# Kernel optimization log

Hardware: AMD Instinct MI355X
Metric: run time of the kernel (lower is better)

Reference implementation:

```python
import jax, jax.numpy as jnp
import numpy as np

B, S, H = 4, 2048, 512
I = 1024  # intermediate_dim
E = 8     # num_experts
K = 2     # top_k


def setup_inputs() -> dict:
    key = jax.random.key(0)
    k1, k2, k3, k4 = jax.random.split(key, 4)
    x = jax.random.normal(k1, (B, S, H), dtype=jnp.float32)
    expert_indices = jax.random.randint(k2, (B, S, K), 0, E, dtype=jnp.int32)
    # parameters: init.normal_(std=0.02)
    w13 = 0.02 * jax.random.normal(k3, (E, H, 2 * I), dtype=jnp.float32)
    w2 = 0.02 * jax.random.normal(k4, (E, I, H), dtype=jnp.float32)
    return {"x": x, "expert_indices": expert_indices, "w13": w13, "w2": w2}


def reference(x, expert_indices, w13, w2):
    # x: (B,S,H); expert_indices: (B,S,K); w13: (E,H,2I); w2: (E,I,H)
    # Same math as torch's per-token weight gather + matmul, expressed as
    # dense all-expert GEMM followed by per-token expert selection.
    h13_all = jnp.einsum('bsh,ehd->bsed', x, w13)          # (B,S,E,2I)
    h13 = jnp.take_along_axis(h13_all, expert_indices[..., None], axis=2)  # (B,S,K,2I)
    gate, up = jnp.split(h13, 2, axis=-1)                   # each (B,S,K,I)
    h_inter = jax.nn.silu(gate) * up                        # (B,S,K,I)
    out_all = jnp.einsum('bski,eih->bskeh', h_inter, w2)    # (B,S,K,E,H)
    out = jnp.take_along_axis(out_all, expert_indices[..., None, None], axis=3)
    return out.squeeze(3)                                   # (B,S,K,H)
```

## Files before the change

kernel.cpp:

```cpp
#include <hip/hip_runtime.h>


#define H_DIM 512
#define I_DIM 1024
#define E_NUM 8
#define P_PAIRS 16384
#define CAP P_PAIRS
#define MAX_TILES 136

#define PREP_TW13 2048
#define PREP_TW2 1024
#define PREP_CVT 2048
#define PREP_ROUTE 64
#define PREP_BLOCKS (PREP_TW13 + PREP_TW2 + PREP_CVT + PREP_ROUTE)

typedef _Float16 half8 __attribute__((ext_vector_type(8)));
typedef _Float16 half4 __attribute__((ext_vector_type(4)));
typedef float f32x4 __attribute__((ext_vector_type(4)));
typedef unsigned int u32;
typedef const __attribute__((address_space(1))) u32* gas_t;
typedef __attribute__((address_space(3))) u32* las_t;

__device__ __forceinline__ void glds16(const void* g, void* l) {
  __builtin_amdgcn_global_load_lds((gas_t)g, (las_t)l, 16, 0, 0);
}

__device__ __forceinline__ bool tile_decode(const int* counts, int ty, int& e,
                                            int& m0, int& ne, int& rb) {
  int base = 0;
  rb = 0;
  for (e = 0; e < E_NUM; ++e) {
    ne = counts[e];
    const int nt = (ne + 127) >> 7;
    if (ty < base + nt) { m0 = (ty - base) << 7; return true; }
    base += nt;
    rb += ne;
  }
  return false;
}

__global__ __launch_bounds__(256) void prep_k(
    const float* __restrict__ x, const int* __restrict__ idx,
    const float* __restrict__ w13, const float* __restrict__ w2,
    int* __restrict__ counts, int* __restrict__ lists,
    _Float16* __restrict__ xh, _Float16* __restrict__ w13t,
    _Float16* __restrict__ w2t) {
  __shared__ __align__(16) _Float16 tile[64][68];
  const int b = blockIdx.x;
  const int tid = threadIdx.x;

  if (b < PREP_TW13 + PREP_TW2) {
    const float* src;
    _Float16* dst;
    int R, C, c0, r0;
    if (b < PREP_TW13) {
      R = H_DIM; C = 2 * I_DIM;
      const int e = b >> 8;
      c0 = (b & 31) * 64;
      r0 = ((b >> 5) & 7) * 64;
      src = w13 + (size_t)e * R * C;
      dst = w13t + (size_t)e * C * R;
    } else {
      const int l = b - PREP_TW13;
      R = I_DIM; C = H_DIM;
      const int e = l >> 7;
      c0 = (l & 7) * 64;
      r0 = ((l >> 3) & 15) * 64;
      src = w2 + (size_t)e * R * C;
      dst = w2t + (size_t)e * C * R;
    }
    {
      const int c4 = (tid & 15) * 4;
      const int r4 = (tid >> 4) * 4;
      f32x4 v[4];
      for (int i = 0; i < 4; ++i)
        v[i] = *(const f32x4*)(src + (size_t)(r0 + r4 + i) * C + c0 + c4);
      for (int j = 0; j < 4; ++j) {
        half4 hv = {(_Float16)v[0][j], (_Float16)v[1][j],
                    (_Float16)v[2][j], (_Float16)v[3][j]};
        *(half4*)&tile[c4 + j][r4] = hv;
      }
    }
    __syncthreads();
    {
      const int c = tid >> 3;
      const int r8 = (tid & 7) * 8;
      for (int pass = 0; pass < 2; ++pass) {
        const int col = pass * 32 + c;
        half4 lo = *(const half4*)&tile[col][r8];
        half4 hi = *(const half4*)&tile[col][r8 + 4];
        half8 h = {lo[0], lo[1], lo[2], lo[3], hi[0], hi[1], hi[2], hi[3]};
        *(half8*)(dst + (size_t)(c0 + col) * R + r0 + r8) = h;
      }
    }
  } else if (b < PREP_TW13 + PREP_TW2 + PREP_CVT) {
    const int l = b - (PREP_TW13 + PREP_TW2);
    const size_t i = ((size_t)l * 256 + tid) * 8;
    f32x4 v0 = *(const f32x4*)(x + i);
    f32x4 v1 = *(const f32x4*)(x + i + 4);
    half8 h;
    for (int j = 0; j < 4; ++j) { h[j] = (_Float16)v0[j]; h[j + 4] = (_Float16)v1[j]; }
    *(half8*)(xh + i) = h;
  } else {
    int* lcnt = (int*)&tile[0][0];
    int* lbase = lcnt + E_NUM;
    const int l = b - (PREP_TW13 + PREP_TW2 + PREP_CVT);
    if (tid < E_NUM) lcnt[tid] = 0;
    __syncthreads();
    const int p = l * 256 + tid;
    const int e = idx[p];
    const int r = atomicAdd(&lcnt[e], 1);
    __syncthreads();
    if (tid < E_NUM) lbase[tid] = atomicAdd(&counts[tid], lcnt[tid]);
    __syncthreads();
    lists[e * CAP + lbase[e] + r] = p;
  }
}

__global__ __launch_bounds__(256) void gemm1_k(
    const _Float16* __restrict__ xh, const _Float16* __restrict__ w13t,
    const int* __restrict__ counts, const int* __restrict__ lists,
    _Float16* __restrict__ h_ws) {
  int e, m0, ne, rb;
  if (!tile_decode(counts, blockIdx.y, e, m0, ne, rb)) return;
  const int n0 = blockIdx.x * 64;

  __shared__ int rows[128];
  __shared__ __align__(16) _Float16 As[128 * 32];
  __shared__ __align__(16) _Float16 Bgs[64 * 32];
  __shared__ __align__(16) _Float16 Bus[64 * 32];

  const int tid = threadIdx.x;
  if (tid < 128) {
    const int m = m0 + tid;
    rows[tid] = (m < ne) ? lists[e * CAP + m] : -1;
  }
  __syncthreads();

  const int sr = tid >> 2;
  const int s4 = tid & 3;
  const int segoff = ((s4 ^ ((sr >> 1) & 3)) * 8);
  const int pa0 = rows[sr];
  const int pa1 = rows[64 + sr];
  const int t0 = (pa0 >= 0) ? (pa0 >> 1) : 0;
  const int t1 = (pa1 >= 0) ? (pa1 >> 1) : 0;
  const _Float16* ga0 = xh + (size_t)t0 * H_DIM + segoff;
  const _Float16* ga1 = xh + (size_t)t1 * H_DIM + segoff;
  const _Float16* gbg = w13t + ((size_t)e * 2 * I_DIM + n0 + sr) * H_DIM + segoff;
  const _Float16* gbu = gbg + (size_t)I_DIM * H_DIM;
  _Float16* la0 = As + sr * 32 + s4 * 8;
  _Float16* la1 = As + (64 + sr) * 32 + s4 * 8;
  _Float16* lbg = Bgs + sr * 32 + s4 * 8;
  _Float16* lbu = Bus + sr * 32 + s4 * 8;

  const int lane = tid & 63;
  const int wid = tid >> 6;
  const int wm = wid & 1;
  const int wn = wid >> 1;
  const int fm = lane & 15;
  const int q = lane >> 4;
  int aoff[4], boff[2];
  for (int mi = 0; mi < 4; ++mi) {
    const int rA = wm * 64 + mi * 16 + fm;
    aoff[mi] = rA * 32 + ((q ^ ((rA >> 1) & 3)) * 8);
  }
  for (int ni = 0; ni < 2; ++ni) {
    const int cB = wn * 32 + ni * 16 + fm;
    boff[ni] = cB * 32 + ((q ^ ((cB >> 1) & 3)) * 8);
  }

  f32x4 accg[4][2] = {};
  f32x4 accu[4][2] = {};

  for (int k0 = 0; k0 < H_DIM; k0 += 32) {
    glds16(ga0 + k0, la0);
    glds16(ga1 + k0, la1);
    glds16(gbg + k0, lbg);
    glds16(gbu + k0, lbu);
    __syncthreads();

    half8 af[4], bg[2], bu[2];
    for (int mi = 0; mi < 4; ++mi) af[mi] = *(const half8*)&As[aoff[mi]];
    for (int ni = 0; ni < 2; ++ni) {
      bg[ni] = *(const half8*)&Bgs[boff[ni]];
      bu[ni] = *(const half8*)&Bus[boff[ni]];
    }
    for (int mi = 0; mi < 4; ++mi)
      for (int ni = 0; ni < 2; ++ni) {
        accg[mi][ni] = __builtin_amdgcn_mfma_f32_16x16x32_f16(af[mi], bg[ni], accg[mi][ni], 0, 0, 0);
        accu[mi][ni] = __builtin_amdgcn_mfma_f32_16x16x32_f16(af[mi], bu[ni], accu[mi][ni], 0, 0, 0);
      }
    __syncthreads();
  }

  for (int mi = 0; mi < 4; ++mi)
    for (int r = 0; r < 4; ++r) {
      const int mrow = wm * 64 + mi * 16 + q * 4 + r;
      if (m0 + mrow >= ne) continue;
      _Float16* hrow = h_ws + (size_t)(rb + m0 + mrow) * I_DIM + n0;
      for (int ni = 0; ni < 2; ++ni) {
        const int c = wn * 32 + ni * 16 + fm;
        const float g = accg[mi][ni][r];
        const float u = accu[mi][ni][r];
        hrow[c] = (_Float16)(g / (1.0f + __expf(-g)) * u);
      }
    }
}

__global__ __launch_bounds__(256) void gemm2_k(
    const _Float16* __restrict__ h_ws, const _Float16* __restrict__ w2t,
    const int* __restrict__ counts, const int* __restrict__ lists,
    float* __restrict__ out) {
  int e, m0, ne, rb;
  if (!tile_decode(counts, blockIdx.x, e, m0, ne, rb)) return;
  const int n0 = blockIdx.y * 64;

  __shared__ int rows[128];
  __shared__ __align__(16) _Float16 As[2][128 * 64];
  __shared__ __align__(16) _Float16 Bs[2][64 * 64];

  const int tid = threadIdx.x;
  if (tid < 128) {
    const int m = m0 + tid;
    rows[tid] = (m < ne) ? lists[e * CAP + m] : -1;
  }

  const int s8 = tid & 7;
  const int sr8 = tid >> 3;
  const int sw = ((s8 ^ (sr8 & 7)) * 8);
  const _Float16* gA[4];
  int lA[4];
  for (int pa = 0; pa < 4; ++pa) {
    const int m = pa * 32 + sr8;
    int grow = rb + m0 + m;
    if (grow > P_PAIRS - 1) grow = P_PAIRS - 1;
    gA[pa] = h_ws + (size_t)grow * I_DIM + sw;
    lA[pa] = m * 64 + s8 * 8;
  }
  const _Float16* gB[2];
  int lB[2];
  for (int pb = 0; pb < 2; ++pb) {
    const int n = pb * 32 + sr8;
    gB[pb] = w2t + ((size_t)e * H_DIM + n0 + n) * I_DIM + sw;
    lB[pb] = n * 64 + s8 * 8;
  }

  const int lane = tid & 63;
  const int wid = tid >> 6;
  const int wm = wid & 1;
  const int wn = wid >> 1;
  const int fm = lane & 15;
  const int q = lane >> 4;
  int aoff[2][4], boff[2][2];
  for (int ks = 0; ks < 2; ++ks) {
    for (int mi = 0; mi < 4; ++mi) {
      const int rA = wm * 64 + mi * 16 + fm;
      aoff[ks][mi] = rA * 64 + (((ks * 4 + q) ^ (rA & 7)) * 8);
    }
    for (int ni = 0; ni < 2; ++ni) {
      const int cB = wn * 32 + ni * 16 + fm;
      boff[ks][ni] = cB * 64 + (((ks * 4 + q) ^ (cB & 7)) * 8);
    }
  }

  f32x4 acc[4][2] = {};

#define G2_STAGE(buf, k0)                                  \
  do {                                                     \
    for (int pa = 0; pa < 4; ++pa)                         \
      glds16(gA[pa] + (k0), &As[buf][lA[pa]]);             \
    for (int pb = 0; pb < 2; ++pb)                         \
      glds16(gB[pb] + (k0), &Bs[buf][lB[pb]]);             \
  } while (0)

#define G2_COMPUTE(buf)                                                          \
  do {                                                                           \
    for (int ks = 0; ks < 2; ++ks) {                                             \
      half8 af[4], bf[2];                                                        \
      for (int mi = 0; mi < 4; ++mi)                                             \
        af[mi] = *(const half8*)&As[buf][aoff[ks][mi]];                          \
      for (int ni = 0; ni < 2; ++ni)                                             \
        bf[ni] = *(const half8*)&Bs[buf][boff[ks][ni]];                          \
      for (int mi = 0; mi < 4; ++mi)                                             \
        for (int ni = 0; ni < 2; ++ni)                                           \
          acc[mi][ni] = __builtin_amdgcn_mfma_f32_16x16x32_f16(                  \
              af[mi], bf[ni], acc[mi][ni], 0, 0, 0);                             \
    }                                                                            \
  } while (0)

  G2_STAGE(0, 0);
  __syncthreads();
  for (int k0 = 0; k0 < I_DIM; k0 += 128) {
    G2_STAGE(1, k0 + 64);
    G2_COMPUTE(0);
    __syncthreads();
    if (k0 + 128 < I_DIM) G2_STAGE(0, k0 + 128);
    G2_COMPUTE(1);
    __syncthreads();
  }
#undef G2_STAGE
#undef G2_COMPUTE

  for (int mi = 0; mi < 4; ++mi)
    for (int r = 0; r < 4; ++r) {
      const int mrow = wm * 64 + mi * 16 + q * 4 + r;
      const int p = rows[mrow];
      if (p < 0) continue;
      float* orow = out + (size_t)p * H_DIM + n0;
      for (int ni = 0; ni < 2; ++ni)
        orow[wn * 32 + ni * 16 + fm] = acc[mi][ni][r];
    }
}

extern "C" void kernel_launch(void* const* d_in, const int* in_sizes, int n_in,
                              void* d_out, int out_size, void* d_ws, size_t ws_size,
                              hipStream_t stream) {
  const float* x = (const float*)d_in[0];
  const int* idx = (const int*)d_in[1];
  const float* w13 = (const float*)d_in[2];
  const float* w2 = (const float*)d_in[3];

  char* ws = (char*)d_ws;
  int* counts = (int*)ws;
  int* lists = (int*)(ws + 2048);
  const size_t OFF_XH = 2048 + (size_t)E_NUM * CAP * 4;
  const size_t OFF_W13T = OFF_XH + (size_t)P_PAIRS / 2 * H_DIM * 2;
  const size_t OFF_W2T = OFF_W13T + (size_t)E_NUM * 2 * I_DIM * H_DIM * 2;
  const size_t OFF_H = OFF_W2T + (size_t)E_NUM * H_DIM * I_DIM * 2;
  _Float16* xh = (_Float16*)(ws + OFF_XH);
  _Float16* w13t = (_Float16*)(ws + OFF_W13T);
  _Float16* w2t = (_Float16*)(ws + OFF_W2T);
  _Float16* h_ws = (_Float16*)(ws + OFF_H);

  hipMemsetAsync(d_ws, 0, 128, stream);
  prep_k<<<dim3(PREP_BLOCKS), 256, 0, stream>>>(x, idx, w13, w2, counts, lists,
                                                xh, w13t, w2t);
  gemm1_k<<<dim3(I_DIM / 64, MAX_TILES), 256, 0, stream>>>(
      xh, w13t, counts, lists, h_ws);
  gemm2_k<<<dim3(MAX_TILES, H_DIM / 64), 256, 0, stream>>>(
      h_ws, w2t, counts, lists, (float*)d_out);
}
```

Before: 201.1 us.

## Overlap w2 transpose with gemm1 and vectorize epilogue stores via swapped MFMA operands

Moves the w2 fp32-to-fp16 transpose out of the prep kernel and into extra gemm1 blocks, so it runs concurrently with the first expert GEMM instead of on the prep critical path. Swaps the MFMA A/B operands so each lane holds four consecutive output columns. That lets the gemm1 SiLU epilogue write half4 vectors and the gemm2 epilogue write float4 vectors instead of scalar stores. The transpose helper also changes its LDS padding and load pattern. This adds idle extra blocks to gemm1 and some shared memory for the tile buffer, which may reduce occupancy.

```diff
diff --git a/kernel.cpp b/kernel.cpp
--- a/kernel.cpp
+++ b/kernel.cpp
@@ -9,10 +9,13 @@
 #define MAX_TILES 136
 
 #define PREP_TW13 2048
-#define PREP_TW2 1024
 #define PREP_CVT 2048
 #define PREP_ROUTE 64
-#define PREP_BLOCKS (PREP_TW13 + PREP_TW2 + PREP_CVT + PREP_ROUTE)
+#define PREP_BLOCKS (PREP_TW13 + PREP_CVT + PREP_ROUTE)
+
+#define G1_NX 16
+#define G1_TW2X 8
+#define TW2_BLOCKS 1024
 
 typedef _Float16 half8 __attribute__((ext_vector_type(8)));
 typedef _Float16 half4 __attribute__((ext_vector_type(4)));
@@ -39,62 +42,46 @@
   return false;
 }
 
+__device__ __forceinline__ void transpose64(const float* src, _Float16* dst,
+                                            int R, int C, int r0, int c0,
+                                            int tid, _Float16 (*tile)[72]) {
+  {
+    const int r = tid >> 4;
+    const int c4 = (tid & 15) * 4;
+    for (int pass = 0; pass < 4; ++pass) {
+      f32x4 v = *(const f32x4*)(src + (size_t)(r0 + pass * 16 + r) * C + c0 + c4);
+      for (int j = 0; j < 4; ++j) tile[c4 + j][pass * 16 + r] = (_Float16)v[j];
+    }
+  }
+  __syncthreads();
+  {
+    const int c = tid >> 3;
+    const int r8 = (tid & 7) * 8;
+    for (int pass = 0; pass < 2; ++pass) {
+      half8 h = *(const half8*)&tile[pass * 32 + c][r8];
+      *(half8*)(dst + (size_t)(c0 + pass * 32 + c) * R + r0 + r8) = h;
+    }
+  }
+}
+
 __global__ __launch_bounds__(256) void prep_k(
     const float* __restrict__ x, const int* __restrict__ idx,
-    const float* __restrict__ w13, const float* __restrict__ w2,
+    const float* __restrict__ w13,
     int* __restrict__ counts, int* __restrict__ lists,
-    _Float16* __restrict__ xh, _Float16* __restrict__ w13t,
-    _Float16* __restrict__ w2t) {
-  __shared__ __align__(16) _Float16 tile[64][68];
+    _Float16* __restrict__ xh, _Float16* __restrict__ w13t) {
+  __shared__ __align__(16) _Float16 tile[64][72];
   const int b = blockIdx.x;
   const int tid = threadIdx.x;
 
-  if (b < PREP_TW13 + PREP_TW2) {
-    const float* src;
-    _Float16* dst;
-    int R, C, c0, r0;
-    if (b < PREP_TW13) {
-      R = H_DIM; C = 2 * I_DIM;
-      const int e = b >> 8;
-      c0 = (b & 31) * 64;
-      r0 = ((b >> 5) & 7) * 64;
-      src = w13 + (size_t)e * R * C;
-      dst = w13t + (size_t)e * C * R;
-    } else {
-      const int l = b - PREP_TW13;
-      R = I_DIM; C = H_DIM;
-      const int e = l >> 7;
-      c0 = (l & 7) * 64;
-      r0 = ((l >> 3) & 15) * 64;
-      src = w2 + (size_t)e * R * C;
-      dst = w2t + (size_t)e * C * R;
-    }
-    {
-      const int c4 = (tid & 15) * 4;
-      const int r4 = (tid >> 4) * 4;
-      f32x4 v[4];
-      for (int i = 0; i < 4; ++i)
-        v[i] = *(const f32x4*)(src + (size_t)(r0 + r4 + i) * C + c0 + c4);
-      for (int j = 0; j < 4; ++j) {
-        half4 hv = {(_Float16)v[0][j], (_Float16)v[1][j],
-                    (_Float16)v[2][j], (_Float16)v[3][j]};
-        *(half4*)&tile[c4 + j][r4] = hv;
-      }
-    }
-    __syncthreads();
-    {
-      const int c = tid >> 3;
-      const int r8 = (tid & 7) * 8;
-      for (int pass = 0; pass < 2; ++pass) {
-        const int col = pass * 32 + c;
-        half4 lo = *(const half4*)&tile[col][r8];
-        half4 hi = *(const half4*)&tile[col][r8 + 4];
-        half8 h = {lo[0], lo[1], lo[2], lo[3], hi[0], hi[1], hi[2], hi[3]};
-        *(half8*)(dst + (size_t)(c0 + col) * R + r0 + r8) = h;
-      }
-    }
-  } else if (b < PREP_TW13 + PREP_TW2 + PREP_CVT) {
-    const int l = b - (PREP_TW13 + PREP_TW2);
+  if (b < PREP_TW13) {
+    const int R = H_DIM, C = 2 * I_DIM;
+    const int e = b >> 8;
+    const int c0 = (b & 31) * 64;
+    const int r0 = ((b >> 5) & 7) * 64;
+    transpose64(w13 + (size_t)e * R * C, w13t + (size_t)e * C * R,
+                R, C, r0, c0, tid, tile);
+  } else if (b < PREP_TW13 + PREP_CVT) {
+    const int l = b - PREP_TW13;
     const size_t i = ((size_t)l * 256 + tid) * 8;
     f32x4 v0 = *(const f32x4*)(x + i);
     f32x4 v1 = *(const f32x4*)(x + i + 4);
@@ -104,7 +91,7 @@
   } else {
     int* lcnt = (int*)&tile[0][0];
     int* lbase = lcnt + E_NUM;
-    const int l = b - (PREP_TW13 + PREP_TW2 + PREP_CVT);
+    const int l = b - (PREP_TW13 + PREP_CVT);
     if (tid < E_NUM) lcnt[tid] = 0;
     __syncthreads();
     const int p = l * 256 + tid;
@@ -120,17 +107,33 @@
 __global__ __launch_bounds__(256) void gemm1_k(
     const _Float16* __restrict__ xh, const _Float16* __restrict__ w13t,
     const int* __restrict__ counts, const int* __restrict__ lists,
-    _Float16* __restrict__ h_ws) {
-  int e, m0, ne, rb;
-  if (!tile_decode(counts, blockIdx.y, e, m0, ne, rb)) return;
-  const int n0 = blockIdx.x * 64;
-
+    _Float16* __restrict__ h_ws,
+    const float* __restrict__ w2, _Float16* __restrict__ w2t) {
   __shared__ int rows[128];
   __shared__ __align__(16) _Float16 As[128 * 32];
   __shared__ __align__(16) _Float16 Bgs[64 * 32];
   __shared__ __align__(16) _Float16 Bus[64 * 32];
+  __shared__ __align__(16) _Float16 tile[64][72];
 
   const int tid = threadIdx.x;
+
+  if (blockIdx.x >= G1_NX) {
+    const int id = (blockIdx.x - G1_NX) * MAX_TILES + blockIdx.y;
+    if (id >= TW2_BLOCKS) return;
+    const int R = I_DIM, C = H_DIM;
+    const int e = id >> 7;
+    const int l = id & 127;
+    const int c0 = (l & 7) * 64;
+    const int r0 = ((l >> 3) & 15) * 64;
+    transpose64(w2 + (size_t)e * R * C, w2t + (size_t)e * C * R,
+                R, C, r0, c0, tid, tile);
+    return;
+  }
+
+  int e, m0, ne, rb;
+  if (!tile_decode(counts, blockIdx.y, e, m0, ne, rb)) return;
+  const int n0 = blockIdx.x * 64;
+
   if (tid < 128) {
     const int m = m0 + tid;
     rows[tid] = (m < ne) ? lists[e * CAP + m] : -1;
@@ -187,24 +190,26 @@
     }
     for (int mi = 0; mi < 4; ++mi)
       for (int ni = 0; ni < 2; ++ni) {
-        accg[mi][ni] = __builtin_amdgcn_mfma_f32_16x16x32_f16(af[mi], bg[ni], accg[mi][ni], 0, 0, 0);
-        accu[mi][ni] = __builtin_amdgcn_mfma_f32_16x16x32_f16(af[mi], bu[ni], accu[mi][ni], 0, 0, 0);
+        accg[mi][ni] = __builtin_amdgcn_mfma_f32_16x16x32_f16(bg[ni], af[mi], accg[mi][ni], 0, 0, 0);
+        accu[mi][ni] = __builtin_amdgcn_mfma_f32_16x16x32_f16(bu[ni], af[mi], accu[mi][ni], 0, 0, 0);
       }
     __syncthreads();
   }
 
-  for (int mi = 0; mi < 4; ++mi)
-    for (int r = 0; r < 4; ++r) {
-      const int mrow = wm * 64 + mi * 16 + q * 4 + r;
-      if (m0 + mrow >= ne) continue;
-      _Float16* hrow = h_ws + (size_t)(rb + m0 + mrow) * I_DIM + n0;
-      for (int ni = 0; ni < 2; ++ni) {
-        const int c = wn * 32 + ni * 16 + fm;
+  for (int mi = 0; mi < 4; ++mi) {
+    const int mrow = wm * 64 + mi * 16 + fm;
+    if (m0 + mrow >= ne) continue;
+    _Float16* hrow = h_ws + (size_t)(rb + m0 + mrow) * I_DIM + n0;
+    for (int ni = 0; ni < 2; ++ni) {
+      half4 hv;
+      for (int r = 0; r < 4; ++r) {
         const float g = accg[mi][ni][r];
         const float u = accu[mi][ni][r];
-        hrow[c] = (_Float16)(g / (1.0f + __expf(-g)) * u);
+        hv[r] = (_Float16)(g / (1.0f + __expf(-g)) * u);
       }
-    }
+      *(half4*)&hrow[wn * 32 + ni * 16 + q * 4] = hv;
+    }
+  }
 }
 
 __global__ __launch_bounds__(256) void gemm2_k(
@@ -284,7 +289,7 @@
       for (int mi = 0; mi < 4; ++mi)                                             \
         for (int ni = 0; ni < 2; ++ni)                                           \
           acc[mi][ni] = __builtin_amdgcn_mfma_f32_16x16x32_f16(                  \
-              af[mi], bf[ni], acc[mi][ni], 0, 0, 0);                             \
+              bf[ni], af[mi], acc[mi][ni], 0, 0, 0);                             \
     }                                                                            \
   } while (0)
 
@@ -301,15 +306,13 @@
 #undef G2_STAGE
 #undef G2_COMPUTE
 
-  for (int mi = 0; mi < 4; ++mi)
-    for (int r = 0; r < 4; ++r) {
-      const int mrow = wm * 64 + mi * 16 + q * 4 + r;
-      const int p = rows[mrow];
-      if (p < 0) continue;
-      float* orow = out + (size_t)p * H_DIM + n0;
-      for (int ni = 0; ni < 2; ++ni)
-        orow[wn * 32 + ni * 16 + fm] = acc[mi][ni][r];
-    }
+  for (int mi = 0; mi < 4; ++mi) {
+    const int p = rows[wm * 64 + mi * 16 + fm];
+    if (p < 0) continue;
+    float* orow = out + (size_t)p * H_DIM + n0;
+    for (int ni = 0; ni < 2; ++ni)
+      *(f32x4*)&orow[wn * 32 + ni * 16 + q * 4] = acc[mi][ni];
+  }
 }
 
 extern "C" void kernel_launch(void* const* d_in, const int* in_sizes, int n_in,
@@ -333,10 +336,10 @@
   _Float16* h_ws = (_Float16*)(ws + OFF_H);
 
   hipMemsetAsync(d_ws, 0, 128, stream);
-  prep_k<<<dim3(PREP_BLOCKS), 256, 0, stream>>>(x, idx, w13, w2, counts, lists,
-                                                xh, w13t, w2t);
-  gemm1_k<<<dim3(I_DIM / 64, MAX_TILES), 256, 0, stream>>>(
-      xh, w13t, counts, lists, h_ws);
+  prep_k<<<dim3(PREP_BLOCKS), 256, 0, stream>>>(x, idx, w13, counts, lists,
+                                                xh, w13t);
+  gemm1_k<<<dim3(G1_NX + G1_TW2X, MAX_TILES), 256, 0, stream>>>(
+      xh, w13t, counts, lists, h_ws, w2, w2t);
   gemm2_k<<<dim3(MAX_TILES, H_DIM / 64), 256, 0, stream>>>(
       h_ws, w2t, counts, lists, (float*)d_out);
 }
```

Result: slower. 210.1 us (+4.5%).
